# Kernel tuning notes

Measured on AMD Instinct MI355X. Metric: run time of the kernel, lower is better.

## Reference

```python
import jax, jax.numpy as jnp
import numpy as np

H = 128
IN = 5
EPS = 1e-5


def lstm(x, Wih, Whh, bih, bhh):
    # x: [B,T,D]; PyTorch gate order i,f,g,o along 4H axis
    B, T, _ = x.shape
    xW = jnp.einsum('btd,gd->btg', x, Wih) + bih + bhh  # [B,T,4H]
    WhhT = Whh.T

    def step(carry, xt):
        h, c = carry
        g = xt + h @ WhhT
        i, f, gg, o = jnp.split(g, 4, axis=-1)
        i = jax.nn.sigmoid(i)
        f = jax.nn.sigmoid(f)
        gg = jnp.tanh(gg)
        o = jax.nn.sigmoid(o)
        c = f * c + i * gg
        h = o * jnp.tanh(c)
        return (h, c), h

    h0 = jnp.zeros((B, H), x.dtype)
    _, hs = jax.lax.scan(step, (h0, h0), jnp.swapaxes(xW, 0, 1))
    return jnp.swapaxes(hs, 0, 1)  # [B,T,H]


def batchnorm(x, gamma, beta):
    # training-mode BN over (batch, time) per channel; x: [B,T,H]
    mean = jnp.mean(x, axis=(0, 1))
    var = jnp.var(x, axis=(0, 1))
    return (x - mean) * (gamma * jax.lax.rsqrt(var + EPS)) + beta


def forward_one(x, Wih1, Whh1, bih1, bhh1, g1, b1, Wih2, Whh2, bih2, bhh2, g2, b2, fcW, fcb):
    out = lstm(x, Wih1, Whh1, bih1, bhh1)
    out = batchnorm(out, g1, b1)
    # dropout is identity (eval / deterministic reference)
    out = lstm(out, Wih2, Whh2, bih2, bhh2)
    out = batchnorm(out, g2, b2)
    emb = out[:, -1, :] @ fcW.T + fcb  # [B,128]
    norm = jnp.sqrt(jnp.sum(emb * emb, axis=1, keepdims=True))
    return emb / jnp.maximum(norm, 1e-12)  # F.normalize p=2


def setup_inputs() -> dict:
    key = jax.random.key(0)
    ks = jax.random.split(key, 20)
    B, T = 512, 128
    s_in = 1.0 / np.sqrt(H)
    d = {
        'a': jax.random.normal(ks[0], (B, T, IN), jnp.float32),
        'p': jax.random.normal(ks[1], (B, T, IN), jnp.float32),
        'n': jax.random.normal(ks[2], (B, T, IN), jnp.float32),
        'Wih1': jax.random.uniform(ks[3], (4 * H, IN), jnp.float32, -s_in, s_in),
        'Whh1': jax.random.uniform(ks[4], (4 * H, H), jnp.float32, -s_in, s_in),
        'bih1': jax.random.uniform(ks[5], (4 * H,), jnp.float32, -s_in, s_in),
        'bhh1': jax.random.uniform(ks[6], (4 * H,), jnp.float32, -s_in, s_in),
        'g1': jnp.ones((H,), jnp.float32),
        'b1': jnp.zeros((H,), jnp.float32),
        'Wih2': jax.random.uniform(ks[7], (4 * H, H), jnp.float32, -s_in, s_in),
        'Whh2': jax.random.uniform(ks[8], (4 * H, H), jnp.float32, -s_in, s_in),
        'bih2': jax.random.uniform(ks[9], (4 * H,), jnp.float32, -s_in, s_in),
        'bhh2': jax.random.uniform(ks[10], (4 * H,), jnp.float32, -s_in, s_in),
        'g2': jnp.ones((H,), jnp.float32),
        'b2': jnp.zeros((H,), jnp.float32),
        'fcW': jax.random.uniform(ks[11], (H, H), jnp.float32, -s_in, s_in),
        'fcb': jax.random.uniform(ks[12], (H,), jnp.float32, -s_in, s_in),
    }
    return d


def reference(a, p, n, Wih1, Whh1, bih1, bhh1, g1, b1, Wih2, Whh2, bih2, bhh2, g2, b2, fcW, fcb):
    f = lambda x: forward_one(x, Wih1, Whh1, bih1, bhh1, g1, b1, Wih2, Whh2, bih2, bhh2, g2, b2, fcW, fcb)
    return (f(a), f(p), f(n))
```

## Files before the change

kernel.cpp:

```cpp
#include <hip/hip_runtime.h>


typedef __attribute__((ext_vector_type(8))) _Float16 half8;
typedef __attribute__((ext_vector_type(4))) float f32x4;

#define TS 128
#define HID 128
#define NGATE 512
#define INV_N (1.0f/65536.0f)
#define NL2E  -1.4426950408889634f
#define N2L2E -2.8853900817779268f
#define GCLAMP 57.707801635558536f

#define BAR() asm volatile("s_waitcnt lgkmcnt(0)\n\ts_barrier" ::: "memory")

__device__ __forceinline__ float rcpf(float x) { return __builtin_amdgcn_rcpf(x); }
__device__ __forceinline__ float ex2(float x) { return __builtin_amdgcn_exp2f(x); }

__device__ __forceinline__ float lstm_cell(float zi, float zf, float zg, float zo,
                                           float& c) {
  float zgc = __builtin_amdgcn_fmed3f(zg, -GCLAMP, GCLAMP);
  float ei = ex2(zi);
  float ef = ex2(zf);
  float eg = ex2(zgc);
  float eo = ex2(zo);
  float pi = 1.0f + ei, pg = 1.0f + eg, pf = 1.0f + ef;
  float P = pi * pg;
  float rd = rcpf(P * pf);
  float fv = P * rd;
  float ig = (1.0f - eg) * (pf * rd);
  float cc = fv * c + ig;
  c = cc;
  float t2 = __builtin_amdgcn_fmed3f(cc * N2L2E, -GCLAMP, GCLAMP);
  float ec = ex2(t2);
  float hv = (1.0f - ec) * rcpf((1.0f + eo) * (1.0f + ec));
  return hv;
}


__global__ void prep_all(const float* __restrict__ xa, const float* __restrict__ xp,
                         const float* __restrict__ xn,
                         const float* __restrict__ Whh1, const float* __restrict__ Whh2,
                         const float* __restrict__ bih1, const float* __restrict__ bhh1,
                         _Float16* __restrict__ xpad,
                         _Float16* __restrict__ whhT1, _Float16* __restrict__ whhT2,
                         float* __restrict__ b1c) {
  int bid = blockIdx.x, tid = threadIdx.x;
  if (bid < 768) {
    int i = bid * 256 + tid;
    int tile = i >> 11, rem = i & 2047;
    int t = rem >> 4, r = rem & 15;
    int inp = tile >> 5, rloc = (tile & 31) * 16;
    const float* x = (inp == 0) ? xa : ((inp == 1) ? xp : xn);
    const float* row = x + (size_t)(rloc + r) * 640 + t * 5;
    half8 v = {0, 0, 0, 0, 0, 0, 0, 0};
#pragma unroll
    for (int j = 0; j < 5; ++j) v[j] = (_Float16)row[j];
    *(half8*)&xpad[(size_t)i * 8] = v;
  } else if (bid < 832) {
    int i = (bid - 768) * 256 + tid;
    int which = i >> 13, i8 = i & 8191;
    int kq = i8 >> 9, g = i8 & 511;
    int k0 = (kq >> 2) * 32 + (kq & 3) * 8;
    float gs = ((g >> 7) == 2) ? N2L2E : NL2E;
    const float* src = which ? Whh2 : Whh1;
    half8 v;
#pragma unroll
    for (int j = 0; j < 8; ++j) v[j] = (_Float16)(src[(size_t)g * HID + k0 + j] * gs);
    *(half8*)&(which ? whhT2 : whhT1)[(size_t)i8 * 8] = v;
  } else {
    int i = (bid - 832) * 256 + tid;
    float gs = ((i >> 7) == 2) ? N2L2E : NL2E;
    b1c[i] = (bih1[i] + bhh1[i]) * gs;
  }
}

__global__ __launch_bounds__(512, 2) void lstm1_kernel(
    const _Float16* __restrict__ xpad,
    const float* __restrict__ Wih1,
    const float* __restrict__ b1c,
    const _Float16* __restrict__ whhT,
    _Float16* __restrict__ hs1,
    float* __restrict__ s1sum, float* __restrict__ s1sq) {
  const int wg = blockIdx.x;
  const int inp = wg >> 5;
  const int tid = threadIdx.x;
  const int w = tid >> 6;
  const int lane = tid & 63;
  const int l15 = lane & 15;
  const int quad = lane >> 4;
  const int col = w * 16 + l15;

  __shared__ _Float16 hb[2][2048];
  for (int i = tid; i < 4096; i += 512) ((_Float16*)hb)[i] = (_Float16)0.0f;

  const int rbase = (quad * 16 + l15) * 8;
  const int wbase = (w >> 1) * 512 + ((w & 1) * 2 + (l15 >> 3)) * 128 +
                    quad * 32 + (l15 & 7);

  half8 bh[4][4];
#pragma unroll
  for (int kt = 0; kt < 4; ++kt)
#pragma unroll
    for (int gt = 0; gt < 4; ++gt)
      bh[kt][gt] = *(const half8*)&whhT[(size_t)((kt * 4 + quad) * 512 + gt * 128 + col) * 8];

  half8 bx[4];
#pragma unroll
  for (int gt = 0; gt < 4; ++gt) {
    half8 v = {0, 0, 0, 0, 0, 0, 0, 0};
    if (quad == 0) {
      float gs = (gt == 2) ? N2L2E : NL2E;
#pragma unroll
      for (int j = 0; j < 5; ++j) v[j] = (_Float16)(Wih1[(gt * 128 + col) * 5 + j] * gs);
    }
    bx[gt] = v;
  }
  f32x4 biasv[4];
#pragma unroll
  for (int gt = 0; gt < 4; ++gt) {
    float b = b1c[gt * 128 + col];
    biasv[gt][0] = b; biasv[gt][1] = b; biasv[gt][2] = b; biasv[gt][3] = b;
  }

  half8 xp = {0, 0, 0, 0, 0, 0, 0, 0};
  if (quad == 0) xp = *(const half8*)&xpad[((size_t)(wg * TS) * 16 + l15) * 8];

  float c[4] = {0, 0, 0, 0};
  float ssum = 0.0f, ssq = 0.0f;
  _Float16* hs1w = hs1 + (size_t)wg * TS * 2048;

  for (int t = 0; t < TS; ++t) {
    BAR();
    half8 ah[4];
#pragma unroll
    for (int kt = 0; kt < 4; ++kt)
      ah[kt] = *(const half8*)&hb[t & 1][kt * 512 + rbase];
    if (t > 0) {
      float2 cp = *(const float2*)&hb[t & 1][tid * 4];
      *(float2*)&hs1w[(size_t)(t - 1) * 2048 + tid * 4] = cp;
    }
    f32x4 acc[4];
#pragma unroll
    for (int gt = 0; gt < 4; ++gt)
      acc[gt] = __builtin_amdgcn_mfma_f32_16x16x32_f16(xp, bx[gt], biasv[gt], 0, 0, 0);
    if (t + 1 < TS && quad == 0)
      xp = *(const half8*)&xpad[((size_t)(wg * TS + t + 1) * 16 + l15) * 8];
#pragma unroll
    for (int kt = 0; kt < 4; ++kt)
#pragma unroll
      for (int gt = 0; gt < 4; ++gt)
        acc[gt] = __builtin_amdgcn_mfma_f32_16x16x32_f16(ah[kt], bh[kt][gt], acc[gt], 0, 0, 0);
    const int wb = (t + 1) & 1;
    float hv4[4];
#pragma unroll
    for (int r = 0; r < 4; ++r) {
      float hv = lstm_cell(acc[0][r], acc[1][r], acc[2][r], acc[3][r], c[r]);
      hb[wb][wbase + r * 8] = (_Float16)hv;
      hv4[r] = hv;
    }
#pragma unroll
    for (int r = 0; r < 4; ++r) { ssum += hv4[r]; ssq += hv4[r] * hv4[r]; }
  }
  BAR();
  {
    float2 cp = *(const float2*)&hb[0][tid * 4];
    *(float2*)&hs1w[(size_t)(TS - 1) * 2048 + tid * 4] = cp;
  }
  float s = ssum, q = ssq;
  s += __shfl_xor(s, 16); s += __shfl_xor(s, 32);
  q += __shfl_xor(q, 16); q += __shfl_xor(q, 32);
  if (quad == 0) {
    atomicAdd(&s1sum[inp * HID + col], s);
    atomicAdd(&s1sq[inp * HID + col], q);
  }
}

__global__ void mid_kernel(const float* __restrict__ s1sum, const float* __restrict__ s1sq,
                           const float* __restrict__ g1, const float* __restrict__ b1,
                           const float* __restrict__ Wih2,
                           const float* __restrict__ bih2, const float* __restrict__ bhh2,
                           _Float16* __restrict__ w2s, float* __restrict__ bias2eff) {
  int bid = blockIdx.x, tid = threadIdx.x;
  __shared__ float scB[8];
  __shared__ float shL[128];
  if (bid < 96) {
    int i = bid * 256 + tid;
    int inp = i >> 13, i8 = i & 8191;
    int kq = i8 >> 9, g = i8 & 511;
    int k0 = (kq >> 2) * 32 + (kq & 3) * 8;
    if (tid < 8) {
      int k = k0 + tid;
      float m = s1sum[inp * HID + k] * INV_N;
      float v = s1sq[inp * HID + k] * INV_N - m * m;
      scB[tid] = g1[k] * rsqrtf(v + 1e-5f);
    }
    __syncthreads();
    float gs = ((g >> 7) == 2) ? N2L2E : NL2E;
    const float* wr = Wih2 + (size_t)g * HID + k0;
    half8 v;
#pragma unroll
    for (int j = 0; j < 8; ++j) v[j] = (_Float16)(scB[j] * wr[j] * gs);
    *(half8*)&w2s[((size_t)inp * 8192 + i8) * 8] = v;
  } else {
    int i = (bid - 96) * 256 + tid;
    int inp = i >> 9, g = i & 511;
    if (tid < 128) {
      float m = s1sum[inp * HID + tid] * INV_N;
      float v = s1sq[inp * HID + tid] * INV_N - m * m;
      float s = g1[tid] * rsqrtf(v + 1e-5f);
      shL[tid] = b1[tid] - m * s;
    }
    __syncthreads();
    float acc = bih2[g] + bhh2[g];
    for (int h = 0; h < HID; ++h) acc += shL[h] * Wih2[(size_t)g * HID + h];
    float gs = ((g >> 7) == 2) ? N2L2E : NL2E;
    bias2eff[i] = acc * gs;
  }
}

__global__ __launch_bounds__(512, 2) void lstm2_kernel(
    const _Float16* __restrict__ hs1,
    const _Float16* __restrict__ whhT2,
    const _Float16* __restrict__ w2s,
    const float* __restrict__ bias2eff,
    _Float16* __restrict__ h_last,
    float* __restrict__ s2sum, float* __restrict__ s2sq) {
  const int wg = blockIdx.x;
  const int inp = wg >> 5;
  const int gr0 = wg * 16;
  const int tid = threadIdx.x;
  const int w = tid >> 6;
  const int lane = tid & 63;
  const int l15 = lane & 15;
  const int quad = lane >> 4;
  const int col = w * 16 + l15;

  __shared__ _Float16 hb[2][2048];
  for (int i = tid; i < 4096; i += 512) ((_Float16*)hb)[i] = (_Float16)0.0f;

  const int rbase = (quad * 16 + l15) * 8;
  const int wbase = (w >> 1) * 512 + ((w & 1) * 2 + (l15 >> 3)) * 128 +
                    quad * 32 + (l15 & 7);

  const _Float16* w2sI = w2s + (size_t)inp * HID * NGATE;
  half8 bh[4][4], bxw[4][4];
#pragma unroll
  for (int kt = 0; kt < 4; ++kt)
#pragma unroll
    for (int gt = 0; gt < 4; ++gt) {
      size_t gi = (size_t)((kt * 4 + quad) * 512 + gt * 128 + col) * 8;
      bh[kt][gt] = *(const half8*)&whhT2[gi];
      bxw[kt][gt] = *(const half8*)&w2sI[gi];
    }
  f32x4 biasv[4];
#pragma unroll
  for (int gt = 0; gt < 4; ++gt) {
    float b = bias2eff[inp * NGATE + gt * 128 + col];
    biasv[gt][0] = b; biasv[gt][1] = b; biasv[gt][2] = b; biasv[gt][3] = b;
  }

  const _Float16* hg = hs1 + (size_t)wg * TS * 2048;
  half8 a2A[4], a2B[4];
#pragma unroll
  for (int kt = 0; kt < 4; ++kt) {
    a2A[kt] = *(const half8*)&hg[kt * 512 + rbase];
    a2B[kt] = *(const half8*)&hg[(size_t)2048 + kt * 512 + rbase];
  }

  float c[4] = {0, 0, 0, 0};
  float ssum = 0.0f, ssq = 0.0f;

  auto step = [&](int t, half8 (&cur)[4]) {
    BAR();
    half8 ah[4];
#pragma unroll
    for (int kt = 0; kt < 4; ++kt)
      ah[kt] = *(const half8*)&hb[t & 1][kt * 512 + rbase];
    f32x4 acc[4];
#pragma unroll
    for (int gt = 0; gt < 4; ++gt)
      acc[gt] = __builtin_amdgcn_mfma_f32_16x16x32_f16(cur[0], bxw[0][gt], biasv[gt], 0, 0, 0);
#pragma unroll
    for (int kt = 1; kt < 4; ++kt)
#pragma unroll
      for (int gt = 0; gt < 4; ++gt)
        acc[gt] = __builtin_amdgcn_mfma_f32_16x16x32_f16(cur[kt], bxw[kt][gt], acc[gt], 0, 0, 0);
    if (t + 2 < TS) {
#pragma unroll
      for (int kt = 0; kt < 4; ++kt)
        cur[kt] = *(const half8*)&hg[(size_t)(t + 2) * 2048 + kt * 512 + rbase];
    }
#pragma unroll
    for (int kt = 0; kt < 4; ++kt)
#pragma unroll
      for (int gt = 0; gt < 4; ++gt)
        acc[gt] = __builtin_amdgcn_mfma_f32_16x16x32_f16(ah[kt], bh[kt][gt], acc[gt], 0, 0, 0);
    const int wb = (t + 1) & 1;
    float hv4[4];
#pragma unroll
    for (int r = 0; r < 4; ++r) {
      float hv = lstm_cell(acc[0][r], acc[1][r], acc[2][r], acc[3][r], c[r]);
      hb[wb][wbase + r * 8] = (_Float16)hv;
      hv4[r] = hv;
    }
#pragma unroll
    for (int r = 0; r < 4; ++r) { ssum += hv4[r]; ssq += hv4[r] * hv4[r]; }
  };

  for (int t = 0; t < TS; t += 2) {
    step(t, a2A);
    step(t + 1, a2B);
  }

  BAR();
#pragma unroll
  for (int r = 0; r < 4; ++r)
    h_last[(size_t)(gr0 + quad * 4 + r) * HID + col] = hb[0][wbase + r * 8];

  float s = ssum, q = ssq;
  s += __shfl_xor(s, 16); s += __shfl_xor(s, 32);
  q += __shfl_xor(q, 16); q += __shfl_xor(q, 32);
  if (quad == 0) {
    atomicAdd(&s2sum[inp * HID + col], s);
    atomicAdd(&s2sq[inp * HID + col], q);
  }
}

__global__ __launch_bounds__(256, 1) void head_kernel(
    const _Float16* __restrict__ h_last,
    const float* __restrict__ s2sum, const float* __restrict__ s2sq,
    const float* __restrict__ g2, const float* __restrict__ b2,
    const float* __restrict__ fcW, const float* __restrict__ fcb,
    float* __restrict__ out) {
  const int wg = blockIdx.x;
  const int inp = wg >> 5;
  const int gr0 = wg * 16;
  const int tid = threadIdx.x;

  __shared__ float fcwT[128][132];
  __shared__ float bnh[16][132];
  __shared__ float s2[128], sh2[128];
  __shared__ float part[16][16];
  __shared__ float inv[16];

  if (tid < 128) {
    float m = s2sum[inp * HID + tid] * INV_N;
    float v = s2sq[inp * HID + tid] * INV_N - m * m;
    float s = g2[tid] * rsqrtf(v + 1e-5f);
    s2[tid] = s; sh2[tid] = b2[tid] - m * s;
  }
  for (int i = tid; i < 16384; i += 256) {
    int j = i >> 7, h = i & 127;
    fcwT[h][j] = fcW[i];
  }
  __syncthreads();
  {
    int row = tid >> 4, c0 = (tid & 15) * 8;
#pragma unroll
    for (int k = 0; k < 8; ++k) {
      int h = c0 + k;
      bnh[row][h] = (float)h_last[(gr0 + row) * HID + h] * s2[h] + sh2[h];
    }
  }
  __syncthreads();
  const int row = tid >> 4, jl = tid & 15;
  float emb[8];
  float sq = 0.0f;
#pragma unroll
  for (int jj = 0; jj < 8; ++jj) {
    int j = jl + jj * 16;
    float acc = fcb[j];
    for (int h = 0; h < HID; ++h) acc += bnh[row][h] * fcwT[h][j];
    emb[jj] = acc; sq += acc * acc;
  }
  part[row][jl] = sq;
  __syncthreads();
  if (tid < 16) {
    float s = 0.0f;
    for (int k = 0; k < 16; ++k) s += part[tid][k];
    float nrm = sqrtf(s);
    inv[tid] = 1.0f / fmaxf(nrm, 1e-12f);
  }
  __syncthreads();
#pragma unroll
  for (int jj = 0; jj < 8; ++jj)
    out[(gr0 + row) * HID + jl + jj * 16] = emb[jj] * inv[row];
}

extern "C" void kernel_launch(void* const* d_in, const int* in_sizes, int n_in,
                              void* d_out, int out_size, void* d_ws, size_t ws_size,
                              hipStream_t stream) {
  const float* a    = (const float*)d_in[0];
  const float* p    = (const float*)d_in[1];
  const float* nn   = (const float*)d_in[2];
  const float* Wih1 = (const float*)d_in[3];
  const float* Whh1 = (const float*)d_in[4];
  const float* bih1 = (const float*)d_in[5];
  const float* bhh1 = (const float*)d_in[6];
  const float* g1   = (const float*)d_in[7];
  const float* b1   = (const float*)d_in[8];
  const float* Wih2 = (const float*)d_in[9];
  const float* Whh2 = (const float*)d_in[10];
  const float* bih2 = (const float*)d_in[11];
  const float* bhh2 = (const float*)d_in[12];
  const float* g2   = (const float*)d_in[13];
  const float* b2   = (const float*)d_in[14];
  const float* fcW  = (const float*)d_in[15];
  const float* fcb  = (const float*)d_in[16];

  char* ws = (char*)d_ws;
  float* s1sum = (float*)(ws + 0);
  float* s1sq  = s1sum + 384;
  float* s2sum = s1sum + 768;
  float* s2sq  = s1sum + 1152;
  float* b1c      = (float*)(ws + 6144);
  float* bias2eff = (float*)(ws + 8192);
  _Float16* whhT1 = (_Float16*)(ws + 14336);
  _Float16* whhT2 = (_Float16*)(ws + 145408);
  _Float16* w2s   = (_Float16*)(ws + 276480);
  _Float16* hlast = (_Float16*)(ws + 669696);
  _Float16* xpad  = (_Float16*)(ws + 1062912);
  _Float16* hs1   = (_Float16*)(ws + 4208640);

  hipMemsetAsync(ws, 0, 6144, stream);

  prep_all<<<834, 256, 0, stream>>>(a, p, nn, Whh1, Whh2, bih1, bhh1,
                                    xpad, whhT1, whhT2, b1c);
  lstm1_kernel<<<96, 512, 0, stream>>>(xpad, Wih1, b1c, whhT1, hs1, s1sum, s1sq);
  mid_kernel<<<102, 256, 0, stream>>>(s1sum, s1sq, g1, b1, Wih2, bih2, bhh2,
                                      w2s, bias2eff);
  lstm2_kernel<<<96, 512, 0, stream>>>(hs1, whhT2, w2s, bias2eff, hlast, s2sum, s2sq);
  head_kernel<<<96, 256, 0, stream>>>(hlast, s2sum, s2sq, g2, b2, fcW, fcb, (float*)d_out);
}
```

Before: 337.1 us.

## Fuse all five stages into one cooperative kernel with grid syncs

Replaces the memset plus five separate launches (prep, lstm1, mid, lstm2, head) with a single cooperative mega-kernel of 96 blocks that uses grid.sync between phases. Prep work is spread over the 96 blocks with a grid-stride loop, stats are zeroed in-kernel, and the last hidden state is written directly in the final LSTM step. The aim is to remove launch gaps and inter-kernel overhead. In exchange, prep and mid work now run on only 96 blocks instead of many more, and each grid.sync has its own cost.

```diff
diff --git a/kernel.cpp b/kernel.cpp
--- a/kernel.cpp
+++ b/kernel.cpp
@@ -1,4 +1,7 @@
 #include <hip/hip_runtime.h>
+#include <hip/hip_cooperative_groups.h>
+
+namespace cg = cooperative_groups;
 
 
 typedef __attribute__((ext_vector_type(8))) _Float16 half8;
@@ -38,354 +41,329 @@
 }
 
 
-__global__ void prep_all(const float* __restrict__ xa, const float* __restrict__ xp,
-                         const float* __restrict__ xn,
-                         const float* __restrict__ Whh1, const float* __restrict__ Whh2,
-                         const float* __restrict__ bih1, const float* __restrict__ bhh1,
-                         _Float16* __restrict__ xpad,
-                         _Float16* __restrict__ whhT1, _Float16* __restrict__ whhT2,
-                         float* __restrict__ b1c) {
-  int bid = blockIdx.x, tid = threadIdx.x;
-  if (bid < 768) {
-    int i = bid * 256 + tid;
-    int tile = i >> 11, rem = i & 2047;
-    int t = rem >> 4, r = rem & 15;
-    int inp = tile >> 5, rloc = (tile & 31) * 16;
-    const float* x = (inp == 0) ? xa : ((inp == 1) ? xp : xn);
-    const float* row = x + (size_t)(rloc + r) * 640 + t * 5;
-    half8 v = {0, 0, 0, 0, 0, 0, 0, 0};
-#pragma unroll
-    for (int j = 0; j < 5; ++j) v[j] = (_Float16)row[j];
-    *(half8*)&xpad[(size_t)i * 8] = v;
-  } else if (bid < 832) {
-    int i = (bid - 768) * 256 + tid;
-    int which = i >> 13, i8 = i & 8191;
-    int kq = i8 >> 9, g = i8 & 511;
-    int k0 = (kq >> 2) * 32 + (kq & 3) * 8;
-    float gs = ((g >> 7) == 2) ? N2L2E : NL2E;
-    const float* src = which ? Whh2 : Whh1;
-    half8 v;
-#pragma unroll
-    for (int j = 0; j < 8; ++j) v[j] = (_Float16)(src[(size_t)g * HID + k0 + j] * gs);
-    *(half8*)&(which ? whhT2 : whhT1)[(size_t)i8 * 8] = v;
-  } else {
-    int i = (bid - 832) * 256 + tid;
-    float gs = ((i >> 7) == 2) ? N2L2E : NL2E;
-    b1c[i] = (bih1[i] + bhh1[i]) * gs;
-  }
-}
-
-__global__ __launch_bounds__(512, 2) void lstm1_kernel(
-    const _Float16* __restrict__ xpad,
-    const float* __restrict__ Wih1,
-    const float* __restrict__ b1c,
-    const _Float16* __restrict__ whhT,
-    _Float16* __restrict__ hs1,
-    float* __restrict__ s1sum, float* __restrict__ s1sq) {
+__global__ __launch_bounds__(512, 2) void mega_kernel(
+    const float* __restrict__ xa, const float* __restrict__ xpi,
+    const float* __restrict__ xn,
+    const float* __restrict__ Wih1, const float* __restrict__ Whh1,
+    const float* __restrict__ bih1, const float* __restrict__ bhh1,
+    const float* __restrict__ g1, const float* __restrict__ b1,
+    const float* __restrict__ Wih2, const float* __restrict__ Whh2,
+    const float* __restrict__ bih2, const float* __restrict__ bhh2,
+    const float* __restrict__ g2, const float* __restrict__ b2,
+    const float* __restrict__ fcW, const float* __restrict__ fcb,
+    float* __restrict__ out,
+    float* __restrict__ stats, float* __restrict__ b1c,
+    float* __restrict__ bias2eff,
+    _Float16* __restrict__ whhT1, _Float16* __restrict__ whhT2,
+    _Float16* __restrict__ w2s, _Float16* __restrict__ hlast,
+    _Float16* __restrict__ xpad, _Float16* __restrict__ hs1) {
   const int wg = blockIdx.x;
-  const int inp = wg >> 5;
   const int tid = threadIdx.x;
+  const int gtid = wg * 512 + tid;
   const int w = tid >> 6;
   const int lane = tid & 63;
   const int l15 = lane & 15;
   const int quad = lane >> 4;
   const int col = w * 16 + l15;
-
-  __shared__ _Float16 hb[2][2048];
-  for (int i = tid; i < 4096; i += 512) ((_Float16*)hb)[i] = (_Float16)0.0f;
-
-  const int rbase = (quad * 16 + l15) * 8;
-  const int wbase = (w >> 1) * 512 + ((w & 1) * 2 + (l15 >> 3)) * 128 +
-                    quad * 32 + (l15 & 7);
-
-  half8 bh[4][4];
-#pragma unroll
-  for (int kt = 0; kt < 4; ++kt)
-#pragma unroll
-    for (int gt = 0; gt < 4; ++gt)
-      bh[kt][gt] = *(const half8*)&whhT[(size_t)((kt * 4 + quad) * 512 + gt * 128 + col) * 8];
-
-  half8 bx[4];
-#pragma unroll
-  for (int gt = 0; gt < 4; ++gt) {
-    half8 v = {0, 0, 0, 0, 0, 0, 0, 0};
+  const int inp = wg >> 5;
+
+  __shared__ __align__(16) char smraw[79168];
+  cg::grid_group grid = cg::this_grid();
+
+  {
+    for (int i = gtid; i < 196608; i += 49152) {
+      int tile = i >> 11, rem = i & 2047;
+      int t = rem >> 4, r = rem & 15;
+      int ip = tile >> 5, rloc = (tile & 31) * 16;
+      const float* x = (ip == 0) ? xa : ((ip == 1) ? xpi : xn);
+      const float* row = x + (size_t)(rloc + r) * 640 + t * 5;
+      half8 v = {0, 0, 0, 0, 0, 0, 0, 0};
+#pragma unroll
+      for (int j = 0; j < 5; ++j) v[j] = (_Float16)row[j];
+      *(half8*)&xpad[(size_t)i * 8] = v;
+    }
+    if (gtid < 16384) {
+      int which = gtid >> 13, i8 = gtid & 8191;
+      int kq = i8 >> 9, g = i8 & 511;
+      int k0 = (kq >> 2) * 32 + (kq & 3) * 8;
+      float gs = ((g >> 7) == 2) ? N2L2E : NL2E;
+      const float* src = which ? Whh2 : Whh1;
+      half8 v;
+#pragma unroll
+      for (int j = 0; j < 8; ++j) v[j] = (_Float16)(src[(size_t)g * HID + k0 + j] * gs);
+      *(half8*)&(which ? whhT2 : whhT1)[(size_t)i8 * 8] = v;
+    }
+    if (gtid < 512) {
+      float gs = ((gtid >> 7) == 2) ? N2L2E : NL2E;
+      b1c[gtid] = (bih1[gtid] + bhh1[gtid]) * gs;
+    }
+    if (gtid < 1536) stats[gtid] = 0.0f;
+  }
+  grid.sync();
+
+  {
+    _Float16* hb = (_Float16*)smraw;
+    for (int i = tid; i < 4096; i += 512) hb[i] = (_Float16)0.0f;
+
+    const int rbase = (quad * 16 + l15) * 8;
+    const int wbase = (w >> 1) * 512 + ((w & 1) * 2 + (l15 >> 3)) * 128 +
+                      quad * 32 + (l15 & 7);
+
+    half8 bh[4][4];
+#pragma unroll
+    for (int kt = 0; kt < 4; ++kt)
+#pragma unroll
+      for (int gt = 0; gt < 4; ++gt)
+        bh[kt][gt] = *(const half8*)&whhT1[(size_t)((kt * 4 + quad) * 512 + gt * 128 + col) * 8];
+
+    half8 bx[4];
+#pragma unroll
+    for (int gt = 0; gt < 4; ++gt) {
+      half8 v = {0, 0, 0, 0, 0, 0, 0, 0};
+      if (quad == 0) {
+        float gs = (gt == 2) ? N2L2E : NL2E;
+#pragma unroll
+        for (int j = 0; j < 5; ++j) v[j] = (_Float16)(Wih1[(gt * 128 + col) * 5 + j] * gs);
+      }
+      bx[gt] = v;
+    }
+    f32x4 biasv[4];
+#pragma unroll
+    for (int gt = 0; gt < 4; ++gt) {
+      float b = b1c[gt * 128 + col];
+      biasv[gt][0] = b; biasv[gt][1] = b; biasv[gt][2] = b; biasv[gt][3] = b;
+    }
+
+    half8 xp8 = {0, 0, 0, 0, 0, 0, 0, 0};
+    if (quad == 0) xp8 = *(const half8*)&xpad[((size_t)(wg * TS) * 16 + l15) * 8];
+
+    float c4[4] = {0, 0, 0, 0};
+    float ssum = 0.0f, ssq = 0.0f;
+    _Float16* hs1w = hs1 + (size_t)wg * TS * 2048;
+
+    for (int t = 0; t < TS; ++t) {
+      BAR();
+      half8 ah[4];
+#pragma unroll
+      for (int kt = 0; kt < 4; ++kt)
+        ah[kt] = *(const half8*)&hb[(t & 1) * 2048 + kt * 512 + rbase];
+      if (t > 0) {
+        float2 cp = *(const float2*)&hb[(t & 1) * 2048 + tid * 4];
+        *(float2*)&hs1w[(size_t)(t - 1) * 2048 + tid * 4] = cp;
+      }
+      f32x4 acc[4];
+#pragma unroll
+      for (int gt = 0; gt < 4; ++gt)
+        acc[gt] = __builtin_amdgcn_mfma_f32_16x16x32_f16(xp8, bx[gt], biasv[gt], 0, 0, 0);
+      if (t + 1 < TS && quad == 0)
+        xp8 = *(const half8*)&xpad[((size_t)(wg * TS + t + 1) * 16 + l15) * 8];
+#pragma unroll
+      for (int kt = 0; kt < 4; ++kt)
+#pragma unroll
+        for (int gt = 0; gt < 4; ++gt)
+          acc[gt] = __builtin_amdgcn_mfma_f32_16x16x32_f16(ah[kt], bh[kt][gt], acc[gt], 0, 0, 0);
+      const int wb = (t + 1) & 1;
+      float hv4[4];
+#pragma unroll
+      for (int r = 0; r < 4; ++r) {
+        float hv = lstm_cell(acc[0][r], acc[1][r], acc[2][r], acc[3][r], c4[r]);
+        hb[wb * 2048 + wbase + r * 8] = (_Float16)hv;
+        hv4[r] = hv;
+      }
+#pragma unroll
+      for (int r = 0; r < 4; ++r) { ssum += hv4[r]; ssq += hv4[r] * hv4[r]; }
+    }
+    BAR();
+    {
+      float2 cp = *(const float2*)&hb[tid * 4];
+      *(float2*)&hs1w[(size_t)(TS - 1) * 2048 + tid * 4] = cp;
+    }
+    float s = ssum, q = ssq;
+    s += __shfl_xor(s, 16); s += __shfl_xor(s, 32);
+    q += __shfl_xor(q, 16); q += __shfl_xor(q, 32);
     if (quad == 0) {
-      float gs = (gt == 2) ? N2L2E : NL2E;
-#pragma unroll
-      for (int j = 0; j < 5; ++j) v[j] = (_Float16)(Wih1[(gt * 128 + col) * 5 + j] * gs);
-    }
-    bx[gt] = v;
+      atomicAdd(&stats[inp * HID + col], s);
+      atomicAdd(&stats[384 + inp * HID + col], q);
+    }
   }
-  f32x4 biasv[4];
-#pragma unroll
-  for (int gt = 0; gt < 4; ++gt) {
-    float b = b1c[gt * 128 + col];
-    biasv[gt][0] = b; biasv[gt][1] = b; biasv[gt][2] = b; biasv[gt][3] = b;
+  grid.sync();
+
+  {
+    if (gtid < 24576) {
+      int ip = gtid >> 13, i8 = gtid & 8191;
+      int kq = i8 >> 9, g = i8 & 511;
+      int k0 = (kq >> 2) * 32 + (kq & 3) * 8;
+      float gs = ((g >> 7) == 2) ? N2L2E : NL2E;
+      const float* wr = Wih2 + (size_t)g * HID + k0;
+      half8 v;
+#pragma unroll
+      for (int j = 0; j < 8; ++j) {
+        int k = k0 + j;
+        float m = stats[ip * HID + k] * INV_N;
+        float vv = stats[384 + ip * HID + k] * INV_N - m * m;
+        float sc = g1[k] * rsqrtf(vv + 1e-5f);
+        v[j] = (_Float16)(sc * wr[j] * gs);
+      }
+      *(half8*)&w2s[(size_t)gtid * 8] = v;
+    } else if (gtid < 26112) {
+      int i = gtid - 24576;
+      int ip = i >> 9, g = i & 511;
+      float acc = bih2[g] + bhh2[g];
+      const float* wr = Wih2 + (size_t)g * HID;
+      for (int h = 0; h < HID; ++h) {
+        float m = stats[ip * HID + h] * INV_N;
+        float vv = stats[384 + ip * HID + h] * INV_N - m * m;
+        float s = g1[h] * rsqrtf(vv + 1e-5f);
+        acc += (b1[h] - m * s) * wr[h];
+      }
+      float gs = ((g >> 7) == 2) ? N2L2E : NL2E;
+      bias2eff[i] = acc * gs;
+    }
   }
-
-  half8 xp = {0, 0, 0, 0, 0, 0, 0, 0};
-  if (quad == 0) xp = *(const half8*)&xpad[((size_t)(wg * TS) * 16 + l15) * 8];
-
-  float c[4] = {0, 0, 0, 0};
-  float ssum = 0.0f, ssq = 0.0f;
-  _Float16* hs1w = hs1 + (size_t)wg * TS * 2048;
-
-  for (int t = 0; t < TS; ++t) {
-    BAR();
-    half8 ah[4];
+  grid.sync();
+
+  {
+    _Float16* hb = (_Float16*)smraw;
+    for (int i = tid; i < 4096; i += 512) hb[i] = (_Float16)0.0f;
+
+    const int gr0 = wg * 16;
+    const int rbase = (quad * 16 + l15) * 8;
+    const int wbase = (w >> 1) * 512 + ((w & 1) * 2 + (l15 >> 3)) * 128 +
+                      quad * 32 + (l15 & 7);
+
+    const _Float16* w2sI = w2s + (size_t)inp * HID * NGATE;
+    half8 bh[4][4], bxw[4][4];
 #pragma unroll
     for (int kt = 0; kt < 4; ++kt)
-      ah[kt] = *(const half8*)&hb[t & 1][kt * 512 + rbase];
-    if (t > 0) {
-      float2 cp = *(const float2*)&hb[t & 1][tid * 4];
-      *(float2*)&hs1w[(size_t)(t - 1) * 2048 + tid * 4] = cp;
-    }
-    f32x4 acc[4];
-#pragma unroll
-    for (int gt = 0; gt < 4; ++gt)
-      acc[gt] = __builtin_amdgcn_mfma_f32_16x16x32_f16(xp, bx[gt], biasv[gt], 0, 0, 0);
-    if (t + 1 < TS && quad == 0)
-      xp = *(const half8*)&xpad[((size_t)(wg * TS + t + 1) * 16 + l15) * 8];
-#pragma unroll
-    for (int kt = 0; kt < 4; ++kt)
+#pragma unroll
+      for (int gt = 0; gt < 4; ++gt) {
+        size_t gi = (size_t)((kt * 4 + quad) * 512 + gt * 128 + col) * 8;
+        bh[kt][gt] = *(const half8*)&whhT2[gi];
+        bxw[kt][gt] = *(const half8*)&w2sI[gi];
+      }
+    f32x4 biasv[4];
+#pragma unroll
+    for (int gt = 0; gt < 4; ++gt) {
+      float b = bias2eff[inp * NGATE + gt * 128 + col];
+      biasv[gt][0] = b; biasv[gt][1] = b; biasv[gt][2] = b; biasv[gt][3] = b;
+    }
+
+    const _Float16* hg = hs1 + (size_t)wg * TS * 2048;
+    half8 a2A[4], a2B[4];
+#pragma unroll
+    for (int kt = 0; kt < 4; ++kt) {
+      a2A[kt] = *(const half8*)&hg[kt * 512 + rbase];
+      a2B[kt] = *(const half8*)&hg[(size_t)2048 + kt * 512 + rbase];
+    }
+
+    float c4[4] = {0, 0, 0, 0};
+    float ssum = 0.0f, ssq = 0.0f;
+
+    auto step = [&](int t, half8 (&cur)[4]) {
+      BAR();
+      half8 ah[4];
+#pragma unroll
+      for (int kt = 0; kt < 4; ++kt)
+        ah[kt] = *(const half8*)&hb[(t & 1) * 2048 + kt * 512 + rbase];
+      f32x4 acc[4];
 #pragma unroll
       for (int gt = 0; gt < 4; ++gt)
-        acc[gt] = __builtin_amdgcn_mfma_f32_16x16x32_f16(ah[kt], bh[kt][gt], acc[gt], 0, 0, 0);
-    const int wb = (t + 1) & 1;
-    float hv4[4];
-#pragma unroll
-    for (int r = 0; r < 4; ++r) {
-      float hv = lstm_cell(acc[0][r], acc[1][r], acc[2][r], acc[3][r], c[r]);
-      hb[wb][wbase + r * 8] = (_Float16)hv;
-      hv4[r] = hv;
-    }
-#pragma unroll
-    for (int r = 0; r < 4; ++r) { ssum += hv4[r]; ssq += hv4[r] * hv4[r]; }
+        acc[gt] = __builtin_amdgcn_mfma_f32_16x16x32_f16(cur[0], bxw[0][gt], biasv[gt], 0, 0, 0);
+#pragma unroll
+      for (int kt = 1; kt < 4; ++kt)
+#pragma unroll
+        for (int gt = 0; gt < 4; ++gt)
+          acc[gt] = __builtin_amdgcn_mfma_f32_16x16x32_f16(cur[kt], bxw[kt][gt], acc[gt], 0, 0, 0);
+      if (t + 2 < TS) {
+#pragma unroll
+        for (int kt = 0; kt < 4; ++kt)
+          cur[kt] = *(const half8*)&hg[(size_t)(t + 2) * 2048 + kt * 512 + rbase];
+      }
+#pragma unroll
+      for (int kt = 0; kt < 4; ++kt)
+#pragma unroll
+        for (int gt = 0; gt < 4; ++gt)
+          acc[gt] = __builtin_amdgcn_mfma_f32_16x16x32_f16(ah[kt], bh[kt][gt], acc[gt], 0, 0, 0);
+      const int wb = (t + 1) & 1;
+      float hv4[4];
+#pragma unroll
+      for (int r = 0; r < 4; ++r) {
+        float hv = lstm_cell(acc[0][r], acc[1][r], acc[2][r], acc[3][r], c4[r]);
+        _Float16 hh = (_Float16)hv;
+        hb[wb * 2048 + wbase + r * 8] = hh;
+        hv4[r] = hv;
+        if (t == TS - 1) hlast[(size_t)(gr0 + quad * 4 + r) * HID + col] = hh;
+      }
+#pragma unroll
+      for (int r = 0; r < 4; ++r) { ssum += hv4[r]; ssq += hv4[r] * hv4[r]; }
+    };
+
+    for (int t = 0; t < TS; t += 2) {
+      step(t, a2A);
+      step(t + 1, a2B);
+    }
+
+    float s = ssum, q = ssq;
+    s += __shfl_xor(s, 16); s += __shfl_xor(s, 32);
+    q += __shfl_xor(q, 16); q += __shfl_xor(q, 32);
+    if (quad == 0) {
+      atomicAdd(&stats[768 + inp * HID + col], s);
+      atomicAdd(&stats[1152 + inp * HID + col], q);
+    }
   }
-  BAR();
+  grid.sync();
+
   {
-    float2 cp = *(const float2*)&hb[0][tid * 4];
-    *(float2*)&hs1w[(size_t)(TS - 1) * 2048 + tid * 4] = cp;
+    float* fcwT = (float*)smraw;
+    float* bnh  = fcwT + 128 * 132;
+    float* s2v  = bnh + 16 * 132;
+    float* sh2v = s2v + 128;
+    float* part = sh2v + 128;
+    float* inv  = part + 16 * 32;
+    const int gr0 = wg * 16;
+
+    if (tid < 128) {
+      float m = stats[768 + inp * HID + tid] * INV_N;
+      float v = stats[1152 + inp * HID + tid] * INV_N - m * m;
+      float s = g2[tid] * rsqrtf(v + 1e-5f);
+      s2v[tid] = s; sh2v[tid] = b2[tid] - m * s;
+    }
+    for (int i = tid; i < 16384; i += 512) {
+      int j = i >> 7, h = i & 127;
+      fcwT[h * 132 + j] = fcW[i];
+    }
+    __syncthreads();
+    {
+      int row = tid >> 5, c0 = (tid & 31) * 4;
+#pragma unroll
+      for (int k = 0; k < 4; ++k) {
+        int h = c0 + k;
+        bnh[row * 132 + h] = (float)hlast[(gr0 + row) * HID + h] * s2v[h] + sh2v[h];
+      }
+    }
+    __syncthreads();
+    const int row = tid >> 5, jl = tid & 31;
+    float emb[4];
+    float sq = 0.0f;
+#pragma unroll
+    for (int jj = 0; jj < 4; ++jj) {
+      int j = jl + jj * 32;
+      float acc = fcb[j];
+      for (int h = 0; h < HID; ++h) acc += bnh[row * 132 + h] * fcwT[h * 132 + j];
+      emb[jj] = acc; sq += acc * acc;
+    }
+    part[row * 32 + jl] = sq;
+    __syncthreads();
+    if (tid < 16) {
+      float s = 0.0f;
+      for (int k = 0; k < 32; ++k) s += part[tid * 32 + k];
+      inv[tid] = 1.0f / fmaxf(sqrtf(s), 1e-12f);
+    }
+    __syncthreads();
+#pragma unroll
+    for (int jj = 0; jj < 4; ++jj)
+      out[(gr0 + row) * HID + jl + jj * 32] = emb[jj] * inv[row];
   }
-  float s = ssum, q = ssq;
-  s += __shfl_xor(s, 16); s += __shfl_xor(s, 32);
-  q += __shfl_xor(q, 16); q += __shfl_xor(q, 32);
-  if (quad == 0) {
-    atomicAdd(&s1sum[inp * HID + col], s);
-    atomicAdd(&s1sq[inp * HID + col], q);
-  }
-}
-
-__global__ void mid_kernel(const float* __restrict__ s1sum, const float* __restrict__ s1sq,
-                           const float* __restrict__ g1, const float* __restrict__ b1,
-                           const float* __restrict__ Wih2,
-                           const float* __restrict__ bih2, const float* __restrict__ bhh2,
-                           _Float16* __restrict__ w2s, float* __restrict__ bias2eff) {
-  int bid = blockIdx.x, tid = threadIdx.x;
-  __shared__ float scB[8];
-  __shared__ float shL[128];
-  if (bid < 96) {
-    int i = bid * 256 + tid;
-    int inp = i >> 13, i8 = i & 8191;
-    int kq = i8 >> 9, g = i8 & 511;
-    int k0 = (kq >> 2) * 32 + (kq & 3) * 8;
-    if (tid < 8) {
-      int k = k0 + tid;
-      float m = s1sum[inp * HID + k] * INV_N;
-      float v = s1sq[inp * HID + k] * INV_N - m * m;
-      scB[tid] = g1[k] * rsqrtf(v + 1e-5f);
-    }
-    __syncthreads();
-    float gs = ((g >> 7) == 2) ? N2L2E : NL2E;
-    const float* wr = Wih2 + (size_t)g * HID + k0;
-    half8 v;
-#pragma unroll
-    for (int j = 0; j < 8; ++j) v[j] = (_Float16)(scB[j] * wr[j] * gs);
-    *(half8*)&w2s[((size_t)inp * 8192 + i8) * 8] = v;
-  } else {
-    int i = (bid - 96) * 256 + tid;
-    int inp = i >> 9, g = i & 511;
-    if (tid < 128) {
-      float m = s1sum[inp * HID + tid] * INV_N;
-      float v = s1sq[inp * HID + tid] * INV_N - m * m;
-      float s = g1[tid] * rsqrtf(v + 1e-5f);
-      shL[tid] = b1[tid] - m * s;
-    }
-    __syncthreads();
-    float acc = bih2[g] + bhh2[g];
-    for (int h = 0; h < HID; ++h) acc += shL[h] * Wih2[(size_t)g * HID + h];
-    float gs = ((g >> 7) == 2) ? N2L2E : NL2E;
-    bias2eff[i] = acc * gs;
-  }
-}
-
-__global__ __launch_bounds__(512, 2) void lstm2_kernel(
-    const _Float16* __restrict__ hs1,
-    const _Float16* __restrict__ whhT2,
-    const _Float16* __restrict__ w2s,
-    const float* __restrict__ bias2eff,
-    _Float16* __restrict__ h_last,
-    float* __restrict__ s2sum, float* __restrict__ s2sq) {
-  const int wg = blockIdx.x;
-  const int inp = wg >> 5;
-  const int gr0 = wg * 16;
-  const int tid = threadIdx.x;
-  const int w = tid >> 6;
-  const int lane = tid & 63;
-  const int l15 = lane & 15;
-  const int quad = lane >> 4;
-  const int col = w * 16 + l15;
-
-  __shared__ _Float16 hb[2][2048];
-  for (int i = tid; i < 4096; i += 512) ((_Float16*)hb)[i] = (_Float16)0.0f;
-
-  const int rbase = (quad * 16 + l15) * 8;
-  const int wbase = (w >> 1) * 512 + ((w & 1) * 2 + (l15 >> 3)) * 128 +
-                    quad * 32 + (l15 & 7);
-
-  const _Float16* w2sI = w2s + (size_t)inp * HID * NGATE;
-  half8 bh[4][4], bxw[4][4];
-#pragma unroll
-  for (int kt = 0; kt < 4; ++kt)
-#pragma unroll
-    for (int gt = 0; gt < 4; ++gt) {
-      size_t gi = (size_t)((kt * 4 + quad) * 512 + gt * 128 + col) * 8;
-      bh[kt][gt] = *(const half8*)&whhT2[gi];
-      bxw[kt][gt] = *(const half8*)&w2sI[gi];
-    }
-  f32x4 biasv[4];
-#pragma unroll
-  for (int gt = 0; gt < 4; ++gt) {
-    float b = bias2eff[inp * NGATE + gt * 128 + col];
-    biasv[gt][0] = b; biasv[gt][1] = b; biasv[gt][2] = b; biasv[gt][3] = b;
-  }
-
-  const _Float16* hg = hs1 + (size_t)wg * TS * 2048;
-  half8 a2A[4], a2B[4];
-#pragma unroll
-  for (int kt = 0; kt < 4; ++kt) {
-    a2A[kt] = *(const half8*)&hg[kt * 512 + rbase];
-    a2B[kt] = *(const half8*)&hg[(size_t)2048 + kt * 512 + rbase];
-  }
-
-  float c[4] = {0, 0, 0, 0};
-  float ssum = 0.0f, ssq = 0.0f;
-
-  auto step = [&](int t, half8 (&cur)[4]) {
-    BAR();
-    half8 ah[4];
-#pragma unroll
-    for (int kt = 0; kt < 4; ++kt)
-      ah[kt] = *(const half8*)&hb[t & 1][kt * 512 + rbase];
-    f32x4 acc[4];
-#pragma unroll
-    for (int gt = 0; gt < 4; ++gt)
-      acc[gt] = __builtin_amdgcn_mfma_f32_16x16x32_f16(cur[0], bxw[0][gt], biasv[gt], 0, 0, 0);
-#pragma unroll
-    for (int kt = 1; kt < 4; ++kt)
-#pragma unroll
-      for (int gt = 0; gt < 4; ++gt)
-        acc[gt] = __builtin_amdgcn_mfma_f32_16x16x32_f16(cur[kt], bxw[kt][gt], acc[gt], 0, 0, 0);
-    if (t + 2 < TS) {
-#pragma unroll
-      for (int kt = 0; kt < 4; ++kt)
-        cur[kt] = *(const half8*)&hg[(size_t)(t + 2) * 2048 + kt * 512 + rbase];
-    }
-#pragma unroll
-    for (int kt = 0; kt < 4; ++kt)
-#pragma unroll
-      for (int gt = 0; gt < 4; ++gt)
-        acc[gt] = __builtin_amdgcn_mfma_f32_16x16x32_f16(ah[kt], bh[kt][gt], acc[gt], 0, 0, 0);
-    const int wb = (t + 1) & 1;
-    float hv4[4];
-#pragma unroll
-    for (int r = 0; r < 4; ++r) {
-      float hv = lstm_cell(acc[0][r], acc[1][r], acc[2][r], acc[3][r], c[r]);
-      hb[wb][wbase + r * 8] = (_Float16)hv;
-      hv4[r] = hv;
-    }
-#pragma unroll
-    for (int r = 0; r < 4; ++r) { ssum += hv4[r]; ssq += hv4[r] * hv4[r]; }
-  };
-
-  for (int t = 0; t < TS; t += 2) {
-    step(t, a2A);
-    step(t + 1, a2B);
-  }
-
-  BAR();
-#pragma unroll
-  for (int r = 0; r < 4; ++r)
-    h_last[(size_t)(gr0 + quad * 4 + r) * HID + col] = hb[0][wbase + r * 8];
-
-  float s = ssum, q = ssq;
-  s += __shfl_xor(s, 16); s += __shfl_xor(s, 32);
-  q += __shfl_xor(q, 16); q += __shfl_xor(q, 32);
-  if (quad == 0) {
-    atomicAdd(&s2sum[inp * HID + col], s);
-    atomicAdd(&s2sq[inp * HID + col], q);
-  }
-}
-
-__global__ __launch_bounds__(256, 1) void head_kernel(
-    const _Float16* __restrict__ h_last,
-    const float* __restrict__ s2sum, const float* __restrict__ s2sq,
-    const float* __restrict__ g2, const float* __restrict__ b2,
-    const float* __restrict__ fcW, const float* __restrict__ fcb,
-    float* __restrict__ out) {
-  const int wg = blockIdx.x;
-  const int inp = wg >> 5;
-  const int gr0 = wg * 16;
-  const int tid = threadIdx.x;
-
-  __shared__ float fcwT[128][132];
-  __shared__ float bnh[16][132];
-  __shared__ float s2[128], sh2[128];
-  __shared__ float part[16][16];
-  __shared__ float inv[16];
-
-  if (tid < 128) {
-    float m = s2sum[inp * HID + tid] * INV_N;
-    float v = s2sq[inp * HID + tid] * INV_N - m * m;
-    float s = g2[tid] * rsqrtf(v + 1e-5f);
-    s2[tid] = s; sh2[tid] = b2[tid] - m * s;
-  }
-  for (int i = tid; i < 16384; i += 256) {
-    int j = i >> 7, h = i & 127;
-    fcwT[h][j] = fcW[i];
-  }
-  __syncthreads();
-  {
-    int row = tid >> 4, c0 = (tid & 15) * 8;
-#pragma unroll
-    for (int k = 0; k < 8; ++k) {
-      int h = c0 + k;
-      bnh[row][h] = (float)h_last[(gr0 + row) * HID + h] * s2[h] + sh2[h];
-    }
-  }
-  __syncthreads();
-  const int row = tid >> 4, jl = tid & 15;
-  float emb[8];
-  float sq = 0.0f;
-#pragma unroll
-  for (int jj = 0; jj < 8; ++jj) {
-    int j = jl + jj * 16;
-    float acc = fcb[j];
-    for (int h = 0; h < HID; ++h) acc += bnh[row][h] * fcwT[h][j];
-    emb[jj] = acc; sq += acc * acc;
-  }
-  part[row][jl] = sq;
-  __syncthreads();
-  if (tid < 16) {
-    float s = 0.0f;
-    for (int k = 0; k < 16; ++k) s += part[tid][k];
-    float nrm = sqrtf(s);
-    inv[tid] = 1.0f / fmaxf(nrm, 1e-12f);
-  }
-  __syncthreads();
-#pragma unroll
-  for (int jj = 0; jj < 8; ++jj)
-    out[(gr0 + row) * HID + jl + jj * 16] = emb[jj] * inv[row];
 }
 
 extern "C" void kernel_launch(void* const* d_in, const int* in_sizes, int n_in,
@@ -410,10 +388,7 @@
   const float* fcb  = (const float*)d_in[16];
 
   char* ws = (char*)d_ws;
-  float* s1sum = (float*)(ws + 0);
-  float* s1sq  = s1sum + 384;
-  float* s2sum = s1sum + 768;
-  float* s2sq  = s1sum + 1152;
+  float* stats    = (float*)(ws + 0);
   float* b1c      = (float*)(ws + 6144);
   float* bias2eff = (float*)(ws + 8192);
   _Float16* whhT1 = (_Float16*)(ws + 14336);
@@ -422,14 +397,18 @@
   _Float16* hlast = (_Float16*)(ws + 669696);
   _Float16* xpad  = (_Float16*)(ws + 1062912);
   _Float16* hs1   = (_Float16*)(ws + 4208640);
-
-  hipMemsetAsync(ws, 0, 6144, stream);
-
-  prep_all<<<834, 256, 0, stream>>>(a, p, nn, Whh1, Whh2, bih1, bhh1,
-                                    xpad, whhT1, whhT2, b1c);
-  lstm1_kernel<<<96, 512, 0, stream>>>(xpad, Wih1, b1c, whhT1, hs1, s1sum, s1sq);
-  mid_kernel<<<102, 256, 0, stream>>>(s1sum, s1sq, g1, b1, Wih2, bih2, bhh2,
-                                      w2s, bias2eff);
-  lstm2_kernel<<<96, 512, 0, stream>>>(hs1, whhT2, w2s, bias2eff, hlast, s2sum, s2sq);
-  head_kernel<<<96, 256, 0, stream>>>(hlast, s2sum, s2sq, g2, b2, fcW, fcb, (float*)d_out);
+  float* outp = (float*)d_out;
+
+  void* args[] = {
+    (void*)&a, (void*)&p, (void*)&nn,
+    (void*)&Wih1, (void*)&Whh1, (void*)&bih1, (void*)&bhh1,
+    (void*)&g1, (void*)&b1,
+    (void*)&Wih2, (void*)&Whh2, (void*)&bih2, (void*)&bhh2,
+    (void*)&g2, (void*)&b2, (void*)&fcW, (void*)&fcb,
+    (void*)&outp,
+    (void*)&stats, (void*)&b1c, (void*)&bias2eff,
+    (void*)&whhT1, (void*)&whhT2, (void*)&w2s, (void*)&hlast,
+    (void*)&xpad, (void*)&hs1
+  };
+  hipLaunchCooperativeKernel(mega_kernel, dim3(96), dim3(512), args, 0u, stream);
 }
```

Result: slower. 411.7 us (+22.1%).
